# Optimization experiments

Hardware: AMD Instinct MI355X
Metric: run time of the kernel (lower is better)

The kernel has to match this reference:

```python
import jax, jax.numpy as jnp
import numpy as np
import math

_INV_SQRT2 = 1.0 / math.sqrt(2.0)
B, N, D, H = 4, 8192, 1024, 16
DH = D // H  # 64
GH = 4 * DH  # 256


def setup_inputs() -> dict:
    key = jax.random.key(0)
    ks = jax.random.split(key, 8)
    std = 0.02
    return {
        "x": jax.random.normal(ks[0], (B, N, D), jnp.float32),
        "w_q": jax.random.normal(ks[1], (D, D), jnp.float32) * std,
        "w_v": jax.random.normal(ks[2], (D, D), jnp.float32) * std,
        "w_o": jax.random.normal(ks[3], (D, D), jnp.float32) * std,
        "ln_g": jnp.ones((DH,), jnp.float32),
        "ln_b": jnp.zeros((DH,), jnp.float32),
        "gate_w1": jax.random.normal(ks[4], (DH, GH), jnp.float32) * std,
        "gate_w2": jax.random.normal(ks[5], (GH, 2 * N), jnp.float32) * std,
        "wrm_w1": jax.random.normal(ks[6], (DH, GH), jnp.float32) * std,
        "wrm_w2": jax.random.normal(ks[7], (GH, N), jnp.float32) * std,
    }


def reference(x, w_q, w_v, w_o, ln_g, ln_b, gate_w1, gate_w2, wrm_w1, wrm_w2):
    b, n, d = x.shape
    h, dh = H, DH
    # projections -> (b, h, n, dh)
    q = (x @ w_q).reshape(b, n, h, dh).transpose(0, 2, 1, 3)
    v = (x @ w_v).reshape(b, n, h, dh).transpose(0, 2, 1, 3)
    # per-head summary query + LayerNorm (biased variance, eps=1e-5)
    bar_q = q.mean(axis=2)  # (b, h, dh)
    mu = bar_q.mean(axis=-1, keepdims=True)
    var = ((bar_q - mu) ** 2).mean(axis=-1, keepdims=True)
    bar_q = (bar_q - mu) / jnp.sqrt(var + 1e-5) * ln_g + ln_b
    # complex spectral gate: (b, h, 2n) -> real || imag
    g_raw = jax.nn.gelu(bar_q @ gate_w1, approximate=False) @ gate_w2
    g = g_raw[..., :n] + 1j * g_raw[..., n:]  # (b, h, n) complex
    # FFT -> gate -> IFFT along sequence axis
    v_hat = jnp.fft.fft(v, axis=2) * g[..., None]
    v_tilde = jnp.fft.ifft(v_hat, axis=2).real.astype(x.dtype)
    # Haar wavelet refinement
    even, odd = v_tilde[..., 0::2, :], v_tilde[..., 1::2, :]
    w_hat = jnp.concatenate([(even + odd) * _INV_SQRT2,
                             (even - odd) * _INV_SQRT2], axis=-2)
    s = (jax.nn.gelu(bar_q @ wrm_w1, approximate=False) @ wrm_w2)[..., None]
    w_hat = w_hat * s
    half = n // 2
    low, high = w_hat[..., :half, :], w_hat[..., half:, :]
    ev = (low + high) * _INV_SQRT2
    od = (low - high) * _INV_SQRT2
    v_ref = jnp.stack([ev, od], axis=-2).reshape(b, h, n, dh)  # interleave even/odd
    v_tilde = v_tilde + v_ref
    y = v_tilde.transpose(0, 2, 1, 3).reshape(b, n, d)
    return y @ w_o
```

## Files before the change

### kernel.cpp

```cpp
#include <hip/hip_runtime.h>
#include <hip/hip_bf16.h>
#include <math.h>

#define PB 4
#define PN 8192
#define PD 1024
#define PH 16
#define PDH 64
#define PGH 256

typedef __bf16 bf16x8 __attribute__((ext_vector_type(8)));
typedef __bf16 bf16x2 __attribute__((ext_vector_type(2)));
typedef float f32x4 __attribute__((ext_vector_type(4)));
typedef unsigned int u32;
typedef unsigned short u16;

typedef __attribute__((address_space(3))) void lds_void_t;
typedef const __attribute__((address_space(1))) void gbl_void_t;
#define ASYNC_COPY16(gp, lp) \
    __builtin_amdgcn_global_load_lds((gbl_void_t*)(gp), (lds_void_t*)(lp), 16, 0, 0)

__device__ inline float gelu_exact(float x) {
    return 0.5f * x * (1.0f + erff(x * 0.70710678118654752440f));
}

__device__ inline float2 f2(float x, float y) { return make_float2(x, y); }
__device__ inline float2 cadd(float2 a, float2 b) { return f2(a.x + b.x, a.y + b.y); }
__device__ inline float2 csub(float2 a, float2 b) { return f2(a.x - b.x, a.y - b.y); }
__device__ inline float2 cmul(float2 a, float2 b) {
    return f2(a.x * b.x - a.y * b.y, a.x * b.y + a.y * b.x);
}

#define PHYS(i) ((i) ^ (((i) >> 4) & 15))

__device__ inline u32 packbf(float a, float b) {
    __bf16 ba = (__bf16)a, bb = (__bf16)b;
    return (u32)(*(u16*)&ba) | ((u32)(*(u16*)&bb) << 16);
}

__device__ inline void dif4(float2& a, float2& b, float2& c, float2& d,
                            float2 w2, float2 w1) {
    float2 A0 = cadd(a, c);
    float2 C0 = cmul(csub(a, c), w2);
    float2 B0 = cadd(b, d);
    float2 t  = cmul(csub(b, d), w2);
    float2 D0 = f2(t.y, -t.x);
    a = cadd(A0, B0);
    b = cmul(csub(A0, B0), w1);
    c = cadd(C0, D0);
    d = cmul(csub(C0, D0), w1);
}

__device__ inline void dit4(float2& a, float2& b, float2& c, float2& d,
                            float2 w2, float2 w1) {
    float2 tb = cmul(b, w1);
    float2 p0 = cadd(a, tb), p1 = csub(a, tb);
    float2 td = cmul(d, w1);
    float2 q0 = cadd(c, td), q1 = csub(c, td);
    float2 wq0 = cmul(q0, w2);
    float2 e   = cmul(q1, w2);
    float2 ei  = f2(-e.y, e.x);
    a = cadd(p0, wq0);
    c = csub(p0, wq0);
    b = cadd(p1, ei);
    d = csub(p1, ei);
}

template<int S>
__device__ inline void fwd16_layers(float2 X[4][4], int u) {
    const int h4 = 1 << (S - 2);
    const int off = u & (h4 - 1);
    float sn, cs;
    const float ang1 = -6.283185307179586f / (float)(1 << (S + 2));
    __sincosf(ang1 * (float)off, &sn, &cs);
    float2 w2 = f2(cs, sn);
    const float2 c8m = f2(0.92387953251129f, -0.38268343236509f);
    #pragma unroll
    for (int b = 0; b < 4; b++) {
        float2 w1 = cmul(w2, w2);
        dif4(X[0][b], X[1][b], X[2][b], X[3][b], w2, w1);
        w2 = cmul(w2, c8m);
    }
    const float ang2 = -6.283185307179586f / (float)(1 << S);
    __sincosf(ang2 * (float)off, &sn, &cs);
    float2 v2 = f2(cs, sn);
    float2 v1 = cmul(v2, v2);
    #pragma unroll
    for (int a = 0; a < 4; a++)
        dif4(X[a][0], X[a][1], X[a][2], X[a][3], v2, v1);
}

template<int S>
__device__ inline void inv16_layers(float2 X[4][4], int u) {
    const int h = 1 << S;
    const int off = u & (h - 1);
    float sn, cs;
    const float ang1 = 6.283185307179586f / (float)(4 * h);
    __sincosf(ang1 * (float)off, &sn, &cs);
    float2 w2 = f2(cs, sn), w1 = cmul(w2, w2);
    #pragma unroll
    for (int a = 0; a < 4; a++)
        dit4(X[a][0], X[a][1], X[a][2], X[a][3], w2, w1);
    const float ang2 = 6.283185307179586f / (float)(16 * h);
    __sincosf(ang2 * (float)off, &sn, &cs);
    float2 v2 = f2(cs, sn);
    const float2 c8p = f2(0.92387953251129f, 0.38268343236509f);
    #pragma unroll
    for (int b = 0; b < 4; b++) {
        float2 v1 = cmul(v2, v2);
        dit4(X[0][b], X[1][b], X[2][b], X[3][b], v2, v1);
        v2 = cmul(v2, c8p);
    }
}

__device__ inline void r2_shfl(float2 X[4][4], bool ev) {
    #pragma unroll
    for (int a = 0; a < 4; a++)
        #pragma unroll
        for (int b = 0; b < 4; b++) {
            float2 o = f2(__shfl_xor(X[a][b].x, 1, 64), __shfl_xor(X[a][b].y, 1, 64));
            X[a][b] = ev ? cadd(X[a][b], o) : csub(o, X[a][b]);
        }
}

__global__ void convert_reduce(const float* __restrict__ x, __bf16* __restrict__ xb,
                               float* __restrict__ xsum) {
    int b = blockIdx.z;
    int d = blockIdx.y * 256 + threadIdx.x;
    int n0 = blockIdx.x * 256;
    const float* p = x + ((size_t)b * PN + n0) * PD + d;
    __bf16* q = xb + ((size_t)b * PN + n0) * PD + d;
    float s = 0.0f;
    #pragma unroll 4
    for (int i = 0; i < 256; i++) {
        float v = p[(size_t)i * PD];
        s += v;
        q[(size_t)i * PD] = (__bf16)v;
    }
    atomicAdd(&xsum[b * PD + d], s);
}

__global__ void transpose_w(const float* __restrict__ wv, const float* __restrict__ wo,
                            __bf16* __restrict__ wvt, __bf16* __restrict__ wot) {
    __shared__ float t[64][65];
    const float* src = blockIdx.z ? wo : wv;
    __bf16* dst = blockIdx.z ? wot : wvt;
    int r0 = blockIdx.y * 64, c0 = blockIdx.x * 64;
    int lr = threadIdx.x >> 6, lc = threadIdx.x & 63;
    #pragma unroll
    for (int i = 0; i < 16; i++)
        t[lr + 4 * i][lc] = src[(size_t)(r0 + lr + 4 * i) * PD + c0 + lc];
    __syncthreads();
    #pragma unroll
    for (int i = 0; i < 16; i++)
        dst[(size_t)(c0 + lr + 4 * i) * PD + r0 + lc] = (__bf16)t[lc][lr + 4 * i];
}

__global__ void barq_ln(const float* __restrict__ xsum, const float* __restrict__ w_q,
                        const float* __restrict__ ln_g, const float* __restrict__ ln_b,
                        float* __restrict__ bar_ln) {
    int b = blockIdx.y;
    int lane = threadIdx.x & 63;
    int w = threadIdx.x >> 6;
    int c = blockIdx.x * 64 + lane;
    const float* xs = xsum + b * PD + w * 256;
    const float* wq = w_q + (size_t)(w * 256) * PD + c;
    float acc = 0.0f;
    for (int k = 0; k < 256; k++) acc += xs[k] * wq[(size_t)k * PD];
    __shared__ float part[4][64];
    part[w][lane] = acc;
    __syncthreads();
    if (w == 0) {
        float bar = (part[0][lane] + part[1][lane] + part[2][lane] + part[3][lane])
                    * (1.0f / (float)PN);
        float mu = bar;
        for (int o = 32; o > 0; o >>= 1) mu += __shfl_xor(mu, o, 64);
        mu *= (1.0f / 64.0f);
        float d0 = bar - mu;
        float vv = d0 * d0;
        for (int o = 32; o > 0; o >>= 1) vv += __shfl_xor(vv, o, 64);
        vv *= (1.0f / 64.0f);
        bar_ln[b * PD + c] = d0 * rsqrtf(vv + 1e-5f) * ln_g[lane] + ln_b[lane];
    }
}

__global__ void small1(const float* __restrict__ bar_ln, const float* __restrict__ gw1,
                       const float* __restrict__ ww1, float* __restrict__ tg,
                       float* __restrict__ tw) {
    int bh = blockIdx.x;
    int j = threadIdx.x;
    __shared__ float bl[PDH];
    if (j < PDH) bl[j] = bar_ln[bh * PDH + j];
    __syncthreads();
    float a1 = 0.0f, a2 = 0.0f;
    for (int k = 0; k < PDH; k++) {
        float bv = bl[k];
        a1 += bv * gw1[k * PGH + j];
        a2 += bv * ww1[k * PGH + j];
    }
    tg[bh * PGH + j] = gelu_exact(a1);
    tw[bh * PGH + j] = gelu_exact(a2);
}

__global__ void small2(const float* __restrict__ tg, const float* __restrict__ tw,
                       const float* __restrict__ gw2, const float* __restrict__ ww2,
                       float* __restrict__ g_raw, float* __restrict__ s_full) {
    int chunk = blockIdx.x;
    int bh0 = blockIdx.y * 8;
    bool isg = chunk < 64;
    const float* t = isg ? tg : tw;
    const float* w2 = isg ? gw2 : ww2;
    int stride = isg ? (2 * PN) : PN;
    int col = (isg ? chunk : chunk - 64) * 256 + threadIdx.x;
    __shared__ float tl[8][PGH];
    #pragma unroll
    for (int i = 0; i < 8; i++) tl[i][threadIdx.x] = t[(bh0 + i) * PGH + threadIdx.x];
    __syncthreads();
    float acc[8] = {0, 0, 0, 0, 0, 0, 0, 0};
    for (int k = 0; k < PGH; k++) {
        float w = w2[(size_t)k * stride + col];
        #pragma unroll
        for (int i = 0; i < 8; i++) acc[i] += tl[i][k] * w;
    }
    #pragma unroll
    for (int i = 0; i < 8; i++) {
        if (isg) g_raw[(size_t)(bh0 + i) * (2 * PN) + col] = acc[i];
        else     s_full[(size_t)(bh0 + i) * PN + col] = acc[i];
    }
}

__global__ __launch_bounds__(256) void gemm_pair(const __bf16* __restrict__ A,
                                                 const __bf16* __restrict__ Bt,
                                                 u32* __restrict__ vt) {
    constexpr int K = PD, LDK = 32;
    __shared__ __attribute__((aligned(16))) __bf16 As[128 * LDK];
    __shared__ __attribute__((aligned(16))) __bf16 Bs[128 * LDK];
    const int tid = threadIdx.x;
    const int lane = tid & 63;
    const int wave = tid >> 6;
    const int wm = (wave >> 1) << 6;
    const int wn = (wave & 1) << 6;
    const int tileM = blockIdx.y << 7;
    const int tileN = blockIdx.x << 7;
    const int r = tid >> 2;
    const int cg = tid & 3;
    const int mrow = lane & 15;
    const int k0 = (lane >> 4) << 3;

    f32x4 acc[4][4] = {};
    const __bf16* Aptr = A + (size_t)(tileM + r) * K + cg * 8;
    const __bf16* Bptr = Bt + (size_t)(tileN + r) * K + cg * 8;

    for (int kt = 0; kt < K; kt += 32) {
        __syncthreads();
        ASYNC_COPY16(Aptr + kt,                  As + tid * 8);
        ASYNC_COPY16(Aptr + (size_t)64 * K + kt, As + 64 * LDK + tid * 8);
        ASYNC_COPY16(Bptr + kt,                  Bs + tid * 8);
        ASYNC_COPY16(Bptr + (size_t)64 * K + kt, Bs + 64 * LDK + tid * 8);
        __syncthreads();
        bf16x8 af[4], bfr[4];
        #pragma unroll
        for (int i = 0; i < 4; i++) af[i]  = *(const bf16x8*)&As[(wm + i * 16 + mrow) * LDK + k0];
        #pragma unroll
        for (int j = 0; j < 4; j++) bfr[j] = *(const bf16x8*)&Bs[(wn + j * 16 + mrow) * LDK + k0];
        #pragma unroll
        for (int i = 0; i < 4; i++)
            #pragma unroll
            for (int j = 0; j < 4; j++)
                acc[i][j] = __builtin_amdgcn_mfma_f32_16x16x32_bf16(af[i], bfr[j], acc[i][j], 0, 0, 0);
    }

    const int rq = (lane >> 4) << 2;
    const bool evl = (lane & 1) == 0;
    #pragma unroll
    for (int i = 0; i < 4; i++) {
        int grow = tileM + wm + i * 16 + rq;
        int b = grow >> 13;
        int nb = grow & 8191;
        #pragma unroll
        for (int j = 0; j < 4; j++) {
            u32 w[4];
            #pragma unroll
            for (int rr = 0; rr < 4; rr++) {
                float a = acc[i][j][rr];
                float o = __shfl_xor(a, 1, 64);
                w[rr] = packbf(a, o);
            }
            if (evl) {
                int col = tileN + wn + j * 16 + mrow;
                size_t idx = ((size_t)b * 512 + (col >> 1)) * PN + nb;
                *(uint4*)(vt + idx) = make_uint4(w[0], w[1], w[2], w[3]);
            }
        }
    }
}

__global__ __launch_bounds__(256) void gemm_ta(const u32* __restrict__ yt,
                                               const __bf16* __restrict__ Bt,
                                               float* __restrict__ Cf) {
    constexpr int K = PD, Nc = PD, LDKA = 40, LDKB = 32;
    __shared__ __attribute__((aligned(16))) __bf16 As[128 * LDKA];
    __shared__ __attribute__((aligned(16))) __bf16 Bs[128 * LDKB];
    u32* As32 = (u32*)As;
    const int tid = threadIdx.x;
    const int lane = tid & 63;
    const int wave = tid >> 6;
    const int wm = (wave >> 1) << 6;
    const int wn = (wave & 1) << 6;
    const int tileM = blockIdx.y << 7;
    const int tileN = blockIdx.x << 7;
    const int r = tid >> 2;
    const int cg = tid & 3;
    const int mrow = lane & 15;
    const int k0 = (lane >> 4) << 3;
    const int prow = tid & 7;
    const int seg = tid >> 3;

    const int b = tileM >> 13;
    const int n0 = tileM & 8191;
    const u32* abase = yt + ((size_t)b * 512 + prow) * PN + n0 + seg * 4;
    const __bf16* Bptr = Bt + (size_t)(tileN + r) * K + cg * 8;

    f32x4 acc[4][4] = {};
    uint4 pa0 = *(const uint4*)(abase);
    uint4 pa1 = *(const uint4*)(abase + (size_t)8 * PN);

    for (int kt = 0; kt < K; kt += 32) {
        __syncthreads();
        {
            int m0 = seg * 4;
            As32[(m0 + 0) * 20 + prow] = pa0.x;
            As32[(m0 + 1) * 20 + prow] = pa0.y;
            As32[(m0 + 2) * 20 + prow] = pa0.z;
            As32[(m0 + 3) * 20 + prow] = pa0.w;
            As32[(m0 + 0) * 20 + prow + 8] = pa1.x;
            As32[(m0 + 1) * 20 + prow + 8] = pa1.y;
            As32[(m0 + 2) * 20 + prow + 8] = pa1.z;
            As32[(m0 + 3) * 20 + prow + 8] = pa1.w;
        }
        ASYNC_COPY16(Bptr + kt,                  Bs + tid * 8);
        ASYNC_COPY16(Bptr + (size_t)64 * K + kt, Bs + 64 * LDKB + tid * 8);
        if (kt + 32 < K) {
            const u32* nxt = abase + (size_t)((kt >> 1) + 16) * PN;
            pa0 = *(const uint4*)(nxt);
            pa1 = *(const uint4*)(nxt + (size_t)8 * PN);
        }
        __syncthreads();
        bf16x8 af[4], bfr[4];
        #pragma unroll
        for (int i = 0; i < 4; i++) af[i]  = *(const bf16x8*)&As[(wm + i * 16 + mrow) * LDKA + k0];
        #pragma unroll
        for (int j = 0; j < 4; j++) bfr[j] = *(const bf16x8*)&Bs[(wn + j * 16 + mrow) * LDKB + k0];
        #pragma unroll
        for (int i = 0; i < 4; i++)
            #pragma unroll
            for (int j = 0; j < 4; j++)
                acc[i][j] = __builtin_amdgcn_mfma_f32_16x16x32_bf16(af[i], bfr[j], acc[i][j], 0, 0, 0);
    }

    const int rq = (lane >> 4) << 2;
    #pragma unroll
    for (int i = 0; i < 4; i++) {
        #pragma unroll
        for (int rr = 0; rr < 4; rr++) {
            int row = tileM + wm + i * 16 + rq + rr;
            size_t base = (size_t)row * Nc + tileN + wn + mrow;
            #pragma unroll
            for (int j = 0; j < 4; j++) Cf[base + j * 16] = acc[i][j][rr];
        }
    }
}

__global__ __launch_bounds__(512) void fftconv(const u32* __restrict__ vt,
                                               const float* __restrict__ g_raw,
                                               const float* __restrict__ s_full,
                                               u32* __restrict__ yt) {
    __shared__ float2 Z[PN];
    const int tid = threadIdx.x;
    const int row = blockIdx.x;
    const int bh = row >> 5;
    const u32* vp = vt + (size_t)row * PN;
    const bool ev = (tid & 1) == 0;

    {
        float2 X[4][4];
        #pragma unroll
        for (int a = 0; a < 4; a++)
            #pragma unroll
            for (int b = 0; b < 4; b++) {
                u32 pw = vp[tid + a * 2048 + b * 512];
                bf16x2 pp = *(bf16x2*)&pw;
                X[a][b] = f2((float)pp.x, (float)pp.y);
            }
        fwd16_layers<11>(X, tid);
        #pragma unroll
        for (int a = 0; a < 4; a++)
            #pragma unroll
            for (int b = 0; b < 4; b++)
                Z[PHYS(tid + a * 2048 + b * 512)] = X[a][b];
    }
    __syncthreads();

    {
        const int base = ((tid >> 5) << 9) + (tid & 31);
        float2 X[4][4];
        #pragma unroll
        for (int a = 0; a < 4; a++)
            #pragma unroll
            for (int b = 0; b < 4; b++)
                X[a][b] = Z[PHYS(base + a * 128 + b * 32)];
        fwd16_layers<7>(X, tid);
        #pragma unroll
        for (int a = 0; a < 4; a++)
            #pragma unroll
            for (int b = 0; b < 4; b++)
                Z[PHYS(base + a * 128 + b * 32)] = X[a][b];
    }
    __syncthreads();

    {
        const int base = ((tid >> 1) << 5) + (tid & 1);
        float2 X[4][4];
        #pragma unroll
        for (int a = 0; a < 4; a++)
            #pragma unroll
            for (int b = 0; b < 4; b++)
                X[a][b] = Z[PHYS(base + a * 8 + b * 2)];
        fwd16_layers<3>(X, tid);
        r2_shfl(X, ev);
        #pragma unroll
        for (int a = 0; a < 4; a++)
            #pragma unroll
            for (int b = 0; b < 4; b++)
                Z[PHYS(base + a * 8 + b * 2)] = X[a][b];
    }
    __syncthreads();

    {
        const float* gr = g_raw + (size_t)bh * (2 * PN);
        const float* gi = gr + PN;
        for (int m = tid; m < PN / 2 + 1; m += 512) {
            int p  = (m < PN / 2) ? 2 * m : 1;
            int k  = __brev((unsigned)p) >> 19;
            int Nk = (PN - k) & (PN - 1);
            int qd = __brev((unsigned)Nk) >> 19;
            float2 Za = Z[PHYS(p)], Zb = Z[PHYS(qd)];
            float v1r = 0.5f * (Za.x + Zb.x), v1i = 0.5f * (Za.y - Zb.y);
            float v2r = 0.5f * (Za.y + Zb.y), v2i = 0.5f * (Zb.x - Za.x);
            float grk = gr[k],  gik = gi[k];
            float grn = gr[Nk], gin = gi[Nk];
            float y1r  = v1r * grk - v1i * gik, y1i  = v1r * gik + v1i * grk;
            float y2r  = v2r * grk - v2i * gik, y2i  = v2r * gik + v2i * grk;
            float y1nr = v1r * grn + v1i * gin, y1ni = v1r * gin - v1i * grn;
            float y2nr = v2r * grn + v2i * gin, y2ni = v2r * gin - v2i * grn;
            float ys1r = 0.5f * (y1r + y1nr), ys1i = 0.5f * (y1i - y1ni);
            float ys2r = 0.5f * (y2r + y2nr), ys2i = 0.5f * (y2i - y2ni);
            Z[PHYS(p)] = f2(ys1r - ys2i, ys1i + ys2r);
            if (qd != p) Z[PHYS(qd)] = f2(ys1r + ys2i, ys2r - ys1i);
        }
    }
    __syncthreads();

    {
        const int base = ((tid >> 1) << 5) + (tid & 1);
        float2 X[4][4];
        #pragma unroll
        for (int a = 0; a < 4; a++)
            #pragma unroll
            for (int b = 0; b < 4; b++)
                X[a][b] = Z[PHYS(base + a * 8 + b * 2)];
        r2_shfl(X, ev);
        inv16_layers<1>(X, tid);
        #pragma unroll
        for (int a = 0; a < 4; a++)
            #pragma unroll
            for (int b = 0; b < 4; b++)
                Z[PHYS(base + a * 8 + b * 2)] = X[a][b];
    }
    __syncthreads();

    {
        const int base = ((tid >> 5) << 9) + (tid & 31);
        float2 X[4][4];
        #pragma unroll
        for (int a = 0; a < 4; a++)
            #pragma unroll
            for (int b = 0; b < 4; b++)
                X[a][b] = Z[PHYS(base + a * 128 + b * 32)];
        inv16_layers<5>(X, tid);
        #pragma unroll
        for (int a = 0; a < 4; a++)
            #pragma unroll
            for (int b = 0; b < 4; b++)
                Z[PHYS(base + a * 128 + b * 32)] = X[a][b];
    }
    __syncthreads();

    {
        float2 X[4][4];
        #pragma unroll
        for (int a = 0; a < 4; a++)
            #pragma unroll
            for (int b = 0; b < 4; b++)
                X[a][b] = Z[PHYS(tid + a * 2048 + b * 512)];
        inv16_layers<9>(X, tid);
        #pragma unroll
        for (int a = 0; a < 4; a++)
            #pragma unroll
            for (int b = 0; b < 4; b++)
                Z[PHYS(tid + a * 2048 + b * 512)] = X[a][b];
    }
    __syncthreads();

    {
        const float* sp = s_full + (size_t)bh * PN;
        u32* yp = yt + (size_t)row * PN;
        const float inv = 1.0f / (float)PN;
        const float I2 = 0.70710678118654752440f;
        #pragma unroll
        for (int it = 0; it < 2; it++) {
            int nb = tid + it * 512;
            int n0 = nb * 8;
            int np0 = nb * 4;
            u32 ou[8];
            #pragma unroll
            for (int pp = 0; pp < 4; pp++) {
                float2 z0 = Z[PHYS(n0 + 2 * pp)];
                float2 z1 = Z[PHYS(n0 + 2 * pp + 1)];
                float s0  = sp[np0 + pp];
                float s1v = sp[np0 + pp + PN / 2];
                float ax = z0.x * inv, ay = z0.y * inv;
                float bx = z1.x * inv, by = z1.y * inv;
                float wlx = (ax + bx) * I2 * s0, whx = (ax - bx) * I2 * s1v;
                float evx = (wlx + whx) * I2,   odx = (wlx - whx) * I2;
                float wly = (ay + by) * I2 * s0, why = (ay - by) * I2 * s1v;
                float evy = (wly + why) * I2,   ody = (wly - why) * I2;
                ou[2 * pp]     = packbf(ax + evx, ay + evy);
                ou[2 * pp + 1] = packbf(bx + odx, by + ody);
            }
            *(uint4*)(yp + n0)     = make_uint4(ou[0], ou[1], ou[2], ou[3]);
            *(uint4*)(yp + n0 + 4) = make_uint4(ou[4], ou[5], ou[6], ou[7]);
        }
    }
}

extern "C" void kernel_launch(void* const* d_in, const int* in_sizes, int n_in,
                              void* d_out, int out_size, void* d_ws, size_t ws_size,
                              hipStream_t stream) {
    const float* x    = (const float*)d_in[0];
    const float* w_q  = (const float*)d_in[1];
    const float* w_v  = (const float*)d_in[2];
    const float* w_o  = (const float*)d_in[3];
    const float* ln_g = (const float*)d_in[4];
    const float* ln_b = (const float*)d_in[5];
    const float* gw1  = (const float*)d_in[6];
    const float* gw2  = (const float*)d_in[7];
    const float* ww1  = (const float*)d_in[8];
    const float* ww2  = (const float*)d_in[9];
    float* out = (float*)d_out;

    const size_t XE = (size_t)PB * PN * PD;
    __bf16* xb   = (__bf16*)d_ws;
    __bf16* vb   = xb + XE;
    __bf16* wvt  = vb + XE;
    __bf16* wot  = wvt + (size_t)PD * PD;
    float*  xsum = (float*)(wot + (size_t)PD * PD);
    float*  bar  = xsum + PB * PD;
    float*  tg   = bar + PB * PD;
    float*  tw   = tg + 64 * PGH;
    float*  graw = tw + 64 * PGH;
    float*  sful = graw + (size_t)64 * 2 * PN;

    hipMemsetAsync(xsum, 0, PB * PD * sizeof(float), stream);

    convert_reduce<<<dim3(PN / 256, PD / 256, PB), 256, 0, stream>>>(x, xb, xsum);
    transpose_w<<<dim3(16, 16, 2), 256, 0, stream>>>(w_v, w_o, wvt, wot);
    barq_ln<<<dim3(PD / 64, PB), 256, 0, stream>>>(xsum, w_q, ln_g, ln_b, bar);
    small1<<<PB * PH, 256, 0, stream>>>(bar, gw1, ww1, tg, tw);
    small2<<<dim3(96, 8), 256, 0, stream>>>(tg, tw, gw2, ww2, graw, sful);
    gemm_pair<<<dim3(PD / 128, PB * PN / 128), 256, 0, stream>>>(xb, wvt, (u32*)vb);
    fftconv<<<PB * 512, 512, 0, stream>>>((const u32*)vb, graw, sful, (u32*)xb);
    gemm_ta<<<dim3(PD / 128, PB * PN / 128), 256, 0, stream>>>((const u32*)xb, wot, out);
}
```

Before: 724.8 us.

## Restructure FFT kernel to radix-8 passes with 1024 threads per block

The 8192-point FFT in fftconv changes from three radix-16 register passes per direction with 512 threads to four radix-8 passes with 1024 threads, each thread holding 8 complex values instead of 16. This lowers register pressure and doubles the threads per block, aiming to hide LDS and global latency better. In exchange it adds an extra pass with its own LDS round-trip and __syncthreads in each direction, plus extra twiddle work.

```diff
diff --git a/kernel.cpp b/kernel.cpp
--- a/kernel.cpp
+++ b/kernel.cpp
@@ -67,59 +67,57 @@
 }
 
 template<int S>
-__device__ inline void fwd16_layers(float2 X[4][4], int u) {
-    const int h4 = 1 << (S - 2);
-    const int off = u & (h4 - 1);
+__device__ inline void fwd8_layers(float2 X[2][4], int off) {
+    const float ang = -6.283185307179586f / (float)(8 << S);
     float sn, cs;
-    const float ang1 = -6.283185307179586f / (float)(1 << (S + 2));
-    __sincosf(ang1 * (float)off, &sn, &cs);
-    float2 w2 = f2(cs, sn);
-    const float2 c8m = f2(0.92387953251129f, -0.38268343236509f);
+    __sincosf(ang * (float)off, &sn, &cs);
+    float2 t8 = f2(cs, sn);
+    const float2 c4m = f2(0.70710678118654752f, -0.70710678118654752f);
+    float2 T = t8;
     #pragma unroll
     for (int b = 0; b < 4; b++) {
-        float2 w1 = cmul(w2, w2);
-        dif4(X[0][b], X[1][b], X[2][b], X[3][b], w2, w1);
-        w2 = cmul(w2, c8m);
-    }
-    const float ang2 = -6.283185307179586f / (float)(1 << S);
-    __sincosf(ang2 * (float)off, &sn, &cs);
-    float2 v2 = f2(cs, sn);
-    float2 v1 = cmul(v2, v2);
-    #pragma unroll
-    for (int a = 0; a < 4; a++)
-        dif4(X[a][0], X[a][1], X[a][2], X[a][3], v2, v1);
+        float2 u = X[0][b], v = X[1][b];
+        X[0][b] = cadd(u, v);
+        X[1][b] = cmul(csub(u, v), T);
+        T = cmul(T, c4m);
+    }
+    float2 w2 = cmul(t8, t8);
+    float2 w1 = cmul(w2, w2);
+    #pragma unroll
+    for (int c = 0; c < 2; c++)
+        dif4(X[c][0], X[c][1], X[c][2], X[c][3], w2, w1);
 }
 
 template<int S>
-__device__ inline void inv16_layers(float2 X[4][4], int u) {
-    const int h = 1 << S;
-    const int off = u & (h - 1);
+__device__ inline void inv8_layers(float2 X[2][4], int off) {
+    const float ang = 6.283185307179586f / (float)(8 << S);
     float sn, cs;
-    const float ang1 = 6.283185307179586f / (float)(4 * h);
-    __sincosf(ang1 * (float)off, &sn, &cs);
-    float2 w2 = f2(cs, sn), w1 = cmul(w2, w2);
-    #pragma unroll
-    for (int a = 0; a < 4; a++)
-        dit4(X[a][0], X[a][1], X[a][2], X[a][3], w2, w1);
-    const float ang2 = 6.283185307179586f / (float)(16 * h);
-    __sincosf(ang2 * (float)off, &sn, &cs);
-    float2 v2 = f2(cs, sn);
-    const float2 c8p = f2(0.92387953251129f, 0.38268343236509f);
+    __sincosf(ang * (float)off, &sn, &cs);
+    float2 t8 = f2(cs, sn);
+    float2 w2 = cmul(t8, t8);
+    float2 w1 = cmul(w2, w2);
+    #pragma unroll
+    for (int c = 0; c < 2; c++)
+        dit4(X[c][0], X[c][1], X[c][2], X[c][3], w2, w1);
+    const float2 c4p = f2(0.70710678118654752f, 0.70710678118654752f);
+    float2 T = t8;
     #pragma unroll
     for (int b = 0; b < 4; b++) {
-        float2 v1 = cmul(v2, v2);
-        dit4(X[0][b], X[1][b], X[2][b], X[3][b], v2, v1);
-        v2 = cmul(v2, c8p);
-    }
-}
-
-__device__ inline void r2_shfl(float2 X[4][4], bool ev) {
-    #pragma unroll
-    for (int a = 0; a < 4; a++)
+        float2 tb = cmul(X[1][b], T);
+        float2 u = X[0][b];
+        X[0][b] = cadd(u, tb);
+        X[1][b] = csub(u, tb);
+        T = cmul(T, c4p);
+    }
+}
+
+__device__ inline void r2_shfl8(float2 X[2][4], bool ev) {
+    #pragma unroll
+    for (int c = 0; c < 2; c++)
         #pragma unroll
         for (int b = 0; b < 4; b++) {
-            float2 o = f2(__shfl_xor(X[a][b].x, 1, 64), __shfl_xor(X[a][b].y, 1, 64));
-            X[a][b] = ev ? cadd(X[a][b], o) : csub(o, X[a][b]);
+            float2 o = f2(__shfl_xor(X[c][b].x, 1, 64), __shfl_xor(X[c][b].y, 1, 64));
+            X[c][b] = ev ? cadd(X[c][b], o) : csub(o, X[c][b]);
         }
 }
 
@@ -371,10 +369,10 @@
     }
 }
 
-__global__ __launch_bounds__(512) void fftconv(const u32* __restrict__ vt,
-                                               const float* __restrict__ g_raw,
-                                               const float* __restrict__ s_full,
-                                               u32* __restrict__ yt) {
+__global__ __launch_bounds__(1024, 8) void fftconv(const u32* __restrict__ vt,
+                                                   const float* __restrict__ g_raw,
+                                                   const float* __restrict__ s_full,
+                                                   u32* __restrict__ yt) {
     __shared__ float2 Z[PN];
     const int tid = threadIdx.x;
     const int row = blockIdx.x;
@@ -383,63 +381,80 @@
     const bool ev = (tid & 1) == 0;
 
     {
-        float2 X[4][4];
-        #pragma unroll
-        for (int a = 0; a < 4; a++)
+        float2 X[2][4];
+        #pragma unroll
+        for (int c = 0; c < 2; c++)
             #pragma unroll
             for (int b = 0; b < 4; b++) {
-                u32 pw = vp[tid + a * 2048 + b * 512];
+                u32 pw = vp[tid + c * 4096 + b * 1024];
                 bf16x2 pp = *(bf16x2*)&pw;
-                X[a][b] = f2((float)pp.x, (float)pp.y);
+                X[c][b] = f2((float)pp.x, (float)pp.y);
             }
-        fwd16_layers<11>(X, tid);
-        #pragma unroll
-        for (int a = 0; a < 4; a++)
-            #pragma unroll
-            for (int b = 0; b < 4; b++)
-                Z[PHYS(tid + a * 2048 + b * 512)] = X[a][b];
-    }
-    __syncthreads();
-
-    {
-        const int base = ((tid >> 5) << 9) + (tid & 31);
-        float2 X[4][4];
-        #pragma unroll
-        for (int a = 0; a < 4; a++)
-            #pragma unroll
-            for (int b = 0; b < 4; b++)
-                X[a][b] = Z[PHYS(base + a * 128 + b * 32)];
-        fwd16_layers<7>(X, tid);
-        #pragma unroll
-        for (int a = 0; a < 4; a++)
-            #pragma unroll
-            for (int b = 0; b < 4; b++)
-                Z[PHYS(base + a * 128 + b * 32)] = X[a][b];
-    }
-    __syncthreads();
-
-    {
-        const int base = ((tid >> 1) << 5) + (tid & 1);
-        float2 X[4][4];
-        #pragma unroll
-        for (int a = 0; a < 4; a++)
-            #pragma unroll
-            for (int b = 0; b < 4; b++)
-                X[a][b] = Z[PHYS(base + a * 8 + b * 2)];
-        fwd16_layers<3>(X, tid);
-        r2_shfl(X, ev);
-        #pragma unroll
-        for (int a = 0; a < 4; a++)
-            #pragma unroll
-            for (int b = 0; b < 4; b++)
-                Z[PHYS(base + a * 8 + b * 2)] = X[a][b];
+        fwd8_layers<10>(X, tid);
+        #pragma unroll
+        for (int c = 0; c < 2; c++)
+            #pragma unroll
+            for (int b = 0; b < 4; b++)
+                Z[PHYS(tid + c * 4096 + b * 1024)] = X[c][b];
+    }
+    __syncthreads();
+
+    {
+        const int base = ((tid >> 7) << 10) + (tid & 127);
+        float2 X[2][4];
+        #pragma unroll
+        for (int c = 0; c < 2; c++)
+            #pragma unroll
+            for (int b = 0; b < 4; b++)
+                X[c][b] = Z[PHYS(base + c * 512 + b * 128)];
+        fwd8_layers<7>(X, tid & 127);
+        #pragma unroll
+        for (int c = 0; c < 2; c++)
+            #pragma unroll
+            for (int b = 0; b < 4; b++)
+                Z[PHYS(base + c * 512 + b * 128)] = X[c][b];
+    }
+    __syncthreads();
+
+    {
+        const int base = ((tid >> 4) << 7) + (tid & 15);
+        float2 X[2][4];
+        #pragma unroll
+        for (int c = 0; c < 2; c++)
+            #pragma unroll
+            for (int b = 0; b < 4; b++)
+                X[c][b] = Z[PHYS(base + c * 64 + b * 16)];
+        fwd8_layers<4>(X, tid & 15);
+        #pragma unroll
+        for (int c = 0; c < 2; c++)
+            #pragma unroll
+            for (int b = 0; b < 4; b++)
+                Z[PHYS(base + c * 64 + b * 16)] = X[c][b];
+    }
+    __syncthreads();
+
+    {
+        const int base = ((tid >> 1) << 4) + (tid & 1);
+        float2 X[2][4];
+        #pragma unroll
+        for (int c = 0; c < 2; c++)
+            #pragma unroll
+            for (int b = 0; b < 4; b++)
+                X[c][b] = Z[PHYS(base + c * 8 + b * 2)];
+        fwd8_layers<1>(X, tid & 1);
+        r2_shfl8(X, ev);
+        #pragma unroll
+        for (int c = 0; c < 2; c++)
+            #pragma unroll
+            for (int b = 0; b < 4; b++)
+                Z[PHYS(base + c * 8 + b * 2)] = X[c][b];
     }
     __syncthreads();
 
     {
         const float* gr = g_raw + (size_t)bh * (2 * PN);
         const float* gi = gr + PN;
-        for (int m = tid; m < PN / 2 + 1; m += 512) {
+        for (int m = tid; m < PN / 2 + 1; m += 1024) {
             int p  = (m < PN / 2) ? 2 * m : 1;
             int k  = __brev((unsigned)p) >> 19;
             int Nk = (PN - k) & (PN - 1);
@@ -462,53 +477,70 @@
     __syncthreads();
 
     {
-        const int base = ((tid >> 1) << 5) + (tid & 1);
-        float2 X[4][4];
-        #pragma unroll
-        for (int a = 0; a < 4; a++)
-            #pragma unroll
-            for (int b = 0; b < 4; b++)
-                X[a][b] = Z[PHYS(base + a * 8 + b * 2)];
-        r2_shfl(X, ev);
-        inv16_layers<1>(X, tid);
-        #pragma unroll
-        for (int a = 0; a < 4; a++)
-            #pragma unroll
-            for (int b = 0; b < 4; b++)
-                Z[PHYS(base + a * 8 + b * 2)] = X[a][b];
-    }
-    __syncthreads();
-
-    {
-        const int base = ((tid >> 5) << 9) + (tid & 31);
-        float2 X[4][4];
-        #pragma unroll
-        for (int a = 0; a < 4; a++)
-            #pragma unroll
-            for (int b = 0; b < 4; b++)
-                X[a][b] = Z[PHYS(base + a * 128 + b * 32)];
-        inv16_layers<5>(X, tid);
-        #pragma unroll
-        for (int a = 0; a < 4; a++)
-            #pragma unroll
-            for (int b = 0; b < 4; b++)
-                Z[PHYS(base + a * 128 + b * 32)] = X[a][b];
-    }
-    __syncthreads();
-
-    {
-        float2 X[4][4];
-        #pragma unroll
-        for (int a = 0; a < 4; a++)
-            #pragma unroll
-            for (int b = 0; b < 4; b++)
-                X[a][b] = Z[PHYS(tid + a * 2048 + b * 512)];
-        inv16_layers<9>(X, tid);
-        #pragma unroll
-        for (int a = 0; a < 4; a++)
-            #pragma unroll
-            for (int b = 0; b < 4; b++)
-                Z[PHYS(tid + a * 2048 + b * 512)] = X[a][b];
+        const int base = ((tid >> 1) << 4) + (tid & 1);
+        float2 X[2][4];
+        #pragma unroll
+        for (int c = 0; c < 2; c++)
+            #pragma unroll
+            for (int b = 0; b < 4; b++)
+                X[c][b] = Z[PHYS(base + c * 8 + b * 2)];
+        r2_shfl8(X, ev);
+        inv8_layers<1>(X, tid & 1);
+        #pragma unroll
+        for (int c = 0; c < 2; c++)
+            #pragma unroll
+            for (int b = 0; b < 4; b++)
+                Z[PHYS(base + c * 8 + b * 2)] = X[c][b];
+    }
+    __syncthreads();
+
+    {
+        const int base = ((tid >> 4) << 7) + (tid & 15);
+        float2 X[2][4];
+        #pragma unroll
+        for (int c = 0; c < 2; c++)
+            #pragma unroll
+            for (int b = 0; b < 4; b++)
+                X[c][b] = Z[PHYS(base + c * 64 + b * 16)];
+        inv8_layers<4>(X, tid & 15);
+        #pragma unroll
+        for (int c = 0; c < 2; c++)
+            #pragma unroll
+            for (int b = 0; b < 4; b++)
+                Z[PHYS(base + c * 64 + b * 16)] = X[c][b];
+    }
+    __syncthreads();
+
+    {
+        const int base = ((tid >> 7) << 10) + (tid & 127);
+        float2 X[2][4];
+        #pragma unroll
+        for (int c = 0; c < 2; c++)
+            #pragma unroll
+            for (int b = 0; b < 4; b++)
+                X[c][b] = Z[PHYS(base + c * 512 + b * 128)];
+        inv8_layers<7>(X, tid & 127);
+        #pragma unroll
+        for (int c = 0; c < 2; c++)
+            #pragma unroll
+            for (int b = 0; b < 4; b++)
+                Z[PHYS(base + c * 512 + b * 128)] = X[c][b];
+    }
+    __syncthreads();
+
+    {
+        float2 X[2][4];
+        #pragma unroll
+        for (int c = 0; c < 2; c++)
+            #pragma unroll
+            for (int b = 0; b < 4; b++)
+                X[c][b] = Z[PHYS(tid + c * 4096 + b * 1024)];
+        inv8_layers<10>(X, tid);
+        #pragma unroll
+        for (int c = 0; c < 2; c++)
+            #pragma unroll
+            for (int b = 0; b < 4; b++)
+                Z[PHYS(tid + c * 4096 + b * 1024)] = X[c][b];
     }
     __syncthreads();
 
@@ -517,30 +549,27 @@
         u32* yp = yt + (size_t)row * PN;
         const float inv = 1.0f / (float)PN;
         const float I2 = 0.70710678118654752440f;
-        #pragma unroll
-        for (int it = 0; it < 2; it++) {
-            int nb = tid + it * 512;
-            int n0 = nb * 8;
-            int np0 = nb * 4;
-            u32 ou[8];
-            #pragma unroll
-            for (int pp = 0; pp < 4; pp++) {
-                float2 z0 = Z[PHYS(n0 + 2 * pp)];
-                float2 z1 = Z[PHYS(n0 + 2 * pp + 1)];
-                float s0  = sp[np0 + pp];
-                float s1v = sp[np0 + pp + PN / 2];
-                float ax = z0.x * inv, ay = z0.y * inv;
-                float bx = z1.x * inv, by = z1.y * inv;
-                float wlx = (ax + bx) * I2 * s0, whx = (ax - bx) * I2 * s1v;
-                float evx = (wlx + whx) * I2,   odx = (wlx - whx) * I2;
-                float wly = (ay + by) * I2 * s0, why = (ay - by) * I2 * s1v;
-                float evy = (wly + why) * I2,   ody = (wly - why) * I2;
-                ou[2 * pp]     = packbf(ax + evx, ay + evy);
-                ou[2 * pp + 1] = packbf(bx + odx, by + ody);
-            }
-            *(uint4*)(yp + n0)     = make_uint4(ou[0], ou[1], ou[2], ou[3]);
-            *(uint4*)(yp + n0 + 4) = make_uint4(ou[4], ou[5], ou[6], ou[7]);
+        const int nb = tid;
+        const int n0 = nb * 8;
+        const int np0 = nb * 4;
+        u32 ou[8];
+        #pragma unroll
+        for (int pp = 0; pp < 4; pp++) {
+            float2 z0 = Z[PHYS(n0 + 2 * pp)];
+            float2 z1 = Z[PHYS(n0 + 2 * pp + 1)];
+            float s0  = sp[np0 + pp];
+            float s1v = sp[np0 + pp + PN / 2];
+            float ax = z0.x * inv, ay = z0.y * inv;
+            float bx = z1.x * inv, by = z1.y * inv;
+            float wlx = (ax + bx) * I2 * s0, whx = (ax - bx) * I2 * s1v;
+            float evx = (wlx + whx) * I2,   odx = (wlx - whx) * I2;
+            float wly = (ay + by) * I2 * s0, why = (ay - by) * I2 * s1v;
+            float evy = (wly + why) * I2,   ody = (wly - why) * I2;
+            ou[2 * pp]     = packbf(ax + evx, ay + evy);
+            ou[2 * pp + 1] = packbf(bx + odx, by + ody);
         }
+        *(uint4*)(yp + n0)     = make_uint4(ou[0], ou[1], ou[2], ou[3]);
+        *(uint4*)(yp + n0 + 4) = make_uint4(ou[4], ou[5], ou[6], ou[7]);
     }
 }
 
@@ -579,6 +608,6 @@
     small1<<<PB * PH, 256, 0, stream>>>(bar, gw1, ww1, tg, tw);
     small2<<<dim3(96, 8), 256, 0, stream>>>(tg, tw, gw2, ww2, graw, sful);
     gemm_pair<<<dim3(PD / 128, PB * PN / 128), 256, 0, stream>>>(xb, wvt, (u32*)vb);
-    fftconv<<<PB * 512, 512, 0, stream>>>((const u32*)vb, graw, sful, (u32*)xb);
+    fftconv<<<PB * 512, 1024, 0, stream>>>((const u32*)vb, graw, sful, (u32*)xb);
     gemm_ta<<<dim3(PD / 128, PB * PN / 128), 256, 0, stream>>>((const u32*)xb, wot, out);
 }
```

After: 761.5 us. 5.1% more time.
